# Kernel optimization log

Hardware: AMD Instinct MI355X
Metric: run time of the kernel (lower is better)

## Reference

```python
import jax, jax.numpy as jnp
import numpy as np

B, N, D, C = 2048, 1024, 128, 10  # batch, SOM neurons (32x32), feature dim, classes


def setup_inputs() -> dict:
    key = jax.random.key(0)
    k_x, k_y, k_n, k_l = jax.random.split(key, 4)
    x = jax.random.normal(k_x, (B, D), dtype=jnp.float32)
    y = jax.random.uniform(k_y, (B, C), dtype=jnp.float32)  # argmax -> class ids
    neurons = jax.random.normal(k_n, (N, D), dtype=jnp.float32)
    # labels initialized as random one-hot rows, matching torch one_hot(randint)
    lab_ids = jax.random.randint(k_l, (N,), 0, C)
    labels = jax.nn.one_hot(lab_ids, C, dtype=jnp.float32)
    activities = jnp.zeros((N, C), dtype=jnp.float32)
    labels_count = jnp.zeros((C,), dtype=jnp.int64) if jax.config.jax_enable_x64 else jnp.zeros((C,), dtype=jnp.int32)
    sigma = jnp.ones((1,), dtype=jnp.float32) * 1.5
    return {"x": x, "y": y, "neurons": neurons, "labels": labels,
            "activities": activities, "labels_count": labels_count, "sigma": sigma}


def reference(x, y, neurons, labels, activities, labels_count, sigma):
    sig = sigma[0]
    xr = x.reshape(x.shape[0], 1, -1)              # [B,1,D]
    diff = xr - neurons[None, :, :]                # [B,N,D] broadcasted difference
    d2 = jnp.sum(diff * diff, axis=-1)             # [B,N] squared distances
    d = jnp.sqrt(d2)                               # [B,N]
    bmu = jnp.argmin(d2, axis=-1)                  # [B] best-matching unit
    bmu_d2 = jnp.min(d2, axis=-1)                  # [B]
    g_bmu = jnp.exp(-jnp.sqrt(bmu_d2) / sig)       # [B]
    g = jnp.exp(-d / sig)                          # [B,N]
    gb = g_bmu[:, None]                            # [B,1]
    g_norm = jnp.where(gb == 0, jnp.zeros((), g.dtype), g / gb)  # [B,N]
    batch_last = g_norm.T                          # [N,B] (movedim(0,-1))
    cls = jnp.argmax(y, axis=-1)                   # [B] truth classes
    new_activities = activities.at[:, cls].add(batch_last)   # scatter-add over classes
    new_counts = labels_count.at[cls].add(1)
    out = labels[bmu]                              # [B,C] gather per-sample BMU label
    return out, new_activities, new_counts
```

## Files before the change

kernel.cpp:

```cpp
#include <hip/hip_runtime.h>
#include <hip/hip_bf16.h>
#include <hip/hip_fp16.h>
#include <math.h>

#define Bq 2048
#define Nn 1024
#define Dd 128
#define Cc 10
#define MM 16
#define NBLK (Bq / MM)
#define NTH 1024
#define NC (Nn * Cc)
#define PART_HALFS (NBLK * NC)

#define ACT_OFF (Bq * Cc)
#define CNT_OFF (Bq * Cc + Nn * Cc)

#define WS_CLS_BYTE  (PART_HALFS * 2)
#define WS_NBH_BYTE  (((WS_CLS_BYTE + Bq * 4) + 255) & ~255)
#define WS_NS2_BYTE  (WS_NBH_BYTE + 16 * Nn * 16)
#define WS_NEED_BYTES (WS_NS2_BYTE + Nn * 4)

typedef __attribute__((ext_vector_type(8))) short short8;
typedef __attribute__((ext_vector_type(4))) float f32x4;

__device__ __forceinline__ ushort f2bf(float v, float* back) {
    __hip_bfloat16 h = __float2bfloat16(v);
    *back = __bfloat162float(h);
    return *(const ushort*)&h;
}

__global__ __launch_bounds__(256) void som_prep(
    const float* __restrict__ neurons,
    short8* __restrict__ nbh,
    float* __restrict__ ns2)
{
    __shared__ ushort hsh[8][128];
    const int t     = threadIdx.x;
    const int base8 = blockIdx.x * 8;

    const int r = t >> 5;
    const int c = (t * 4) & 127;
    float4 v = *(const float4*)&neurons[(long)(base8 + r) * Dd + c];
    float back, s;
    ushort h0 = f2bf(v.x, &back); s  = back * back;
    ushort h1 = f2bf(v.y, &back); s += back * back;
    ushort h2 = f2bf(v.z, &back); s += back * back;
    ushort h3 = f2bf(v.w, &back); s += back * back;
    hsh[r][c + 0] = h0;
    hsh[r][c + 1] = h1;
    hsh[r][c + 2] = h2;
    hsh[r][c + 3] = h3;

    #pragma unroll
    for (int off = 16; off; off >>= 1) s += __shfl_xor(s, off);
    if ((t & 31) == 0) ns2[base8 + r] = s;
    __syncthreads();

    if (t < 128) {
        int r2 = t >> 4, kb = t & 15;
        short8 H = *(const short8*)&hsh[r2][kb * 8];
        nbh[kb * Nn + base8 + r2] = H;
    }
}

__global__ __launch_bounds__(NTH) void som_dist(
    const float* __restrict__ x,
    const float* __restrict__ y,
    const short8* __restrict__ nbh,
    const float* __restrict__ ns2,
    const float* __restrict__ labels,
    const float* __restrict__ sigma,
    float* __restrict__ out,
    __half* __restrict__ ws_p,
    int*   __restrict__ ws_cls)
{
    __shared__ ushort xsh[MM * 128];
    __shared__ ushort xsl[MM * 128];
    __shared__ float  xs2s[MM];
    __shared__ float  candv[16][MM];
    __shared__ int    candi[16][MM];
    __shared__ float  bmu_d[MM];
    __shared__ int    bmu_i[MM];
    __shared__ int    clss[MM];

    const int t    = threadIdx.x;
    const int b0   = blockIdx.x * MM;
    const int w    = t >> 6;
    const int lane = t & 63;
    const int g    = lane >> 4;
    const int c16  = lane & 15;

    #pragma unroll
    for (int ii = 0; ii < 2; ++ii) {
        int i   = t + ii * 1024;
        int row = i >> 7;
        int k   = i & 127;
        float v = x[(b0 + row) * Dd + k];
        float back; ushort h = f2bf(v, &back);
        float lo = v - back;
        float b2; ushort l = f2bf(lo, &b2);
        int kb  = k >> 3, j = k & 7;
        int idx = row * 128 + ((kb ^ (row & 7)) << 3) + j;
        xsh[idx] = h;
        xsl[idx] = l;
    }

    {
        float v0 = x[(b0 + w) * Dd + lane];
        float v1 = x[(b0 + w) * Dd + lane + 64];
        float s  = fmaf(v0, v0, v1 * v1);
        #pragma unroll
        for (int off = 32; off; off >>= 1) s += __shfl_xor(s, off);
        if (lane == 0) xs2s[w] = s;
    }
    __syncthreads();

    float dvv[4][4];
    float mval[4]; int midx[4];
    #pragma unroll
    for (int r = 0; r < 4; ++r) { mval[r] = 3.4e38f; midx[r] = 0; }

    const int rowa   = c16;
    const int abase  = rowa * 128;
    const int axor   = (rowa & 7);

    #pragma unroll
    for (int ti = 0; ti < 4; ++ti) {
        const int n0 = w * 64 + ti * 16;
        f32x4 acc = {0.f, 0.f, 0.f, 0.f};
        #pragma unroll
        for (int ks = 0; ks < 4; ++ks) {
            const int kb = ks * 4 + g;
            const int ai = abase + ((kb ^ axor) << 3);
            short8 ah = *(const short8*)&xsh[ai];
            short8 al = *(const short8*)&xsl[ai];
            short8 bh = nbh[kb * Nn + n0 + c16];
            acc = __builtin_amdgcn_mfma_f32_16x16x32_bf16(ah, bh, acc, 0, 0, 0);
            acc = __builtin_amdgcn_mfma_f32_16x16x32_bf16(al, bh, acc, 0, 0, 0);
        }
        const float ns2v = ns2[n0 + c16];
        #pragma unroll
        for (int r = 0; r < 4; ++r) {
            float dv = fmaf(-2.f, acc[r], ns2v);
            dvv[ti][r] = dv;
            if (dv < mval[r]) { mval[r] = dv; midx[r] = n0 + c16; }
        }
    }

    #pragma unroll
    for (int r = 0; r < 4; ++r) {
        float bv = mval[r]; int bi = midx[r];
        #pragma unroll
        for (int off = 8; off; off >>= 1) {
            float ov = __shfl_xor(bv, off);
            int   oi = __shfl_xor(bi, off);
            if (ov < bv || (ov == bv && oi < bi)) { bv = ov; bi = oi; }
        }
        if (c16 == 0) { candv[w][g * 4 + r] = bv; candi[w][g * 4 + r] = bi; }
    }
    __syncthreads();

    if (t < MM) {
        float best = candv[0][t]; int bidx = candi[0][t];
        #pragma unroll
        for (int w2 = 1; w2 < 16; ++w2) {
            float v = candv[w2][t]; int i2 = candi[w2][t];
            if (v < best || (v == best && i2 < bidx)) { best = v; bidx = i2; }
        }
        bmu_i[t] = bidx;
        float d2 = xs2s[t] + best;
        bmu_d[t] = sqrtf(d2 > 0.f ? d2 : 0.f);

        const float* yr = y + (long)(b0 + t) * Cc;
        float bvv = yr[0]; int bc = 0;
        #pragma unroll
        for (int c = 1; c < Cc; ++c) { float v = yr[c]; if (v > bvv) { bvv = v; bc = c; } }
        clss[t] = bc;
        ws_cls[b0 + t] = bc;
    }
    __syncthreads();

    if (t < MM * Cc) {
        int b = t / Cc, c = t % Cc;
        out[(b0 + b) * Cc + c] = labels[bmu_i[b] * Cc + c];
    }

    const float inv_sig = 1.f / sigma[0];
    __half* pb = ws_p + (long)blockIdx.x * NC;

    #pragma unroll
    for (int ti = 0; ti < 4; ++ti) {
        const int n0 = w * 64 + ti * 16;
        float sc[Cc];
        #pragma unroll
        for (int c = 0; c < Cc; ++c) sc[c] = 0.f;
        #pragma unroll
        for (int r = 0; r < 4; ++r) {
            int   row = g * 4 + r;
            float d2  = xs2s[row] + dvv[ti][r];
            float d   = sqrtf(d2 > 0.f ? d2 : 0.f);
            float gn  = expf((bmu_d[row] - d) * inv_sig);
            int   cl  = clss[row];
            #pragma unroll
            for (int c = 0; c < Cc; ++c) sc[c] += (cl == c) ? gn : 0.f;
        }
        #pragma unroll
        for (int c = 0; c < Cc; ++c) {
            float v = sc[c];
            v += __shfl_xor(v, 16);
            v += __shfl_xor(v, 32);
            if (g == 0) pb[c * Nn + n0 + c16] = __float2half(v);
        }
    }
}

__global__ __launch_bounds__(256) void som_fin(
    const float* __restrict__ act_in,
    const int*   __restrict__ cnt_in,
    const __half* __restrict__ ws_p,
    const int*   __restrict__ ws_cls,
    float* __restrict__ out)
{
    if (blockIdx.x < 160) {
        const int t  = threadIdx.x;
        const int kc = t & 3;
        const int j  = blockIdx.x * 64 + (t >> 2);
        const int c  = j >> 10;
        const int n  = j & (Nn - 1);
        const __half* p = ws_p + (long)(kc * 32) * NC + j;
        float s = 0.f;
        #pragma unroll 8
        for (int i = 0; i < 32; ++i) s += __half2float(p[(long)i * NC]);
        s += __shfl_down(s, 2);
        s += __shfl_down(s, 1);
        if (kc == 0) out[ACT_OFF + n * Cc + c] = act_in[n * Cc + c] + s;
    } else {
        __shared__ int hist[Cc];
        if (threadIdx.x < Cc) hist[threadIdx.x] = 0;
        __syncthreads();
        for (int b = threadIdx.x; b < Bq; b += 256) atomicAdd(&hist[ws_cls[b]], 1);
        __syncthreads();
        if (threadIdx.x < Cc)
            out[CNT_OFF + threadIdx.x] = (float)(cnt_in[threadIdx.x] + hist[threadIdx.x]);
    }
}

__global__ void som_init(const float* __restrict__ act_in,
                         const int* __restrict__ cnt_in,
                         float* __restrict__ out) {
    int i = blockIdx.x * blockDim.x + threadIdx.x;
    if (i < Nn * Cc) out[ACT_OFF + i] = act_in[i];
    if (i < Cc) out[CNT_OFF + i] = (float)cnt_in[i];
}

__global__ __launch_bounds__(512) void som_main(
    const float* __restrict__ x,
    const float* __restrict__ y,
    const float* __restrict__ neurons,
    const float* __restrict__ labels,
    const float* __restrict__ sigma,
    float* __restrict__ out)
{
    __shared__ float xs[8][Dd];
    __shared__ float d2s[8][Nn];
    __shared__ float bmu_d[8];
    __shared__ int   bmu_i[8];
    __shared__ int   clss[8];

    const int t  = threadIdx.x;
    const int b0 = blockIdx.x * 8;

    for (int i = t; i < 8 * Dd; i += 512)
        xs[i >> 7][i & (Dd - 1)] = x[b0 * Dd + i];
    __syncthreads();

    float acc0[8], acc1[8];
    #pragma unroll
    for (int b = 0; b < 8; ++b) { acc0[b] = 0.f; acc1[b] = 0.f; }

    const float4* nr0 = (const float4*)(neurons + t * Dd);
    const float4* nr1 = (const float4*)(neurons + (t + 512) * Dd);

    #pragma unroll 2
    for (int dc = 0; dc < Dd / 4; ++dc) {
        float4 nv0 = nr0[dc];
        float4 nv1 = nr1[dc];
        #pragma unroll
        for (int b = 0; b < 8; ++b) {
            float4 xv = *(const float4*)&xs[b][dc * 4];
            float d;
            d = xv.x - nv0.x; acc0[b] = fmaf(d, d, acc0[b]);
            d = xv.y - nv0.y; acc0[b] = fmaf(d, d, acc0[b]);
            d = xv.z - nv0.z; acc0[b] = fmaf(d, d, acc0[b]);
            d = xv.w - nv0.w; acc0[b] = fmaf(d, d, acc0[b]);
            d = xv.x - nv1.x; acc1[b] = fmaf(d, d, acc1[b]);
            d = xv.y - nv1.y; acc1[b] = fmaf(d, d, acc1[b]);
            d = xv.z - nv1.z; acc1[b] = fmaf(d, d, acc1[b]);
            d = xv.w - nv1.w; acc1[b] = fmaf(d, d, acc1[b]);
        }
    }

    #pragma unroll
    for (int b = 0; b < 8; ++b) {
        d2s[b][t]       = acc0[b];
        d2s[b][t + 512] = acc1[b];
    }
    __syncthreads();

    {
        const int wv = t >> 6, lane = t & 63;
        float best = 3.4e38f; int bidx = 0;
        #pragma unroll
        for (int i = 0; i < Nn / 64; ++i) {
            int idx = lane + i * 64;
            float v = d2s[wv][idx];
            if (v < best) { best = v; bidx = idx; }
        }
        #pragma unroll
        for (int off = 32; off; off >>= 1) {
            float ov = __shfl_down(best, off);
            int   oi = __shfl_down(bidx, off);
            if (ov < best || (ov == best && oi < bidx)) { best = ov; bidx = oi; }
        }
        if (lane == 0) { bmu_i[wv] = bidx; bmu_d[wv] = sqrtf(best); }
    }

    if (t < 8) {
        const float* yr = y + (long)(b0 + t) * Cc;
        float bv = yr[0]; int bc = 0;
        #pragma unroll
        for (int c = 1; c < Cc; ++c) { float v = yr[c]; if (v > bv) { bv = v; bc = c; } }
        clss[t] = bc;
        atomicAdd(out + CNT_OFF + bc, 1.0f);
    }
    __syncthreads();

    for (int i = t; i < 8 * Cc; i += 512) {
        int b = i / Cc, c = i % Cc;
        out[(long)(b0 + b) * Cc + c] = labels[(long)bmu_i[b] * Cc + c];
    }

    const float sig = sigma[0];
    #pragma unroll
    for (int b = 0; b < 8; ++b) {
        float gb = expf(-bmu_d[b] / sig);
        int   cl = clss[b];
        float g0 = expf(-sqrtf(acc0[b]) / sig);
        float g1 = expf(-sqrtf(acc1[b]) / sig);
        float gn0 = (gb == 0.f) ? 0.f : g0 / gb;
        float gn1 = (gb == 0.f) ? 0.f : g1 / gb;
        atomicAdd(out + ACT_OFF + t * Cc + cl, gn0);
        atomicAdd(out + ACT_OFF + (t + 512) * Cc + cl, gn1);
    }
}

extern "C" void kernel_launch(void* const* d_in, const int* in_sizes, int n_in,
                              void* d_out, int out_size, void* d_ws, size_t ws_size,
                              hipStream_t stream) {
    const float* x       = (const float*)d_in[0];
    const float* y       = (const float*)d_in[1];
    const float* neurons = (const float*)d_in[2];
    const float* labels  = (const float*)d_in[3];
    const float* act     = (const float*)d_in[4];
    const int*   cnt     = (const int*)d_in[5];
    const float* sigma   = (const float*)d_in[6];
    float* out = (float*)d_out;

    if (ws_size >= (size_t)WS_NEED_BYTES) {
        char*   wsb    = (char*)d_ws;
        __half* ws_p   = (__half*)wsb;
        int*    ws_cls = (int*)(wsb + WS_CLS_BYTE);
        short8* ws_nbh = (short8*)(wsb + WS_NBH_BYTE);
        float*  ws_ns2 = (float*)(wsb + WS_NS2_BYTE);
        som_prep<<<128, 256, 0, stream>>>(neurons, ws_nbh, ws_ns2);
        som_dist<<<NBLK, NTH, 0, stream>>>(x, y, ws_nbh, ws_ns2, labels, sigma, out, ws_p, ws_cls);
        som_fin<<<161, 256, 0, stream>>>(act, cnt, ws_p, ws_cls, out);
    } else {
        som_init<<<(Nn * Cc + 255) / 256, 256, 0, stream>>>(act, cnt, out);
        som_main<<<Bq / 8, 512, 0, stream>>>(x, y, neurons, labels, sigma, out);
    }
}
```

Measured before the change: 30.16 us.

## Fuse prep, distance and reduction kernels into one launch with grid barriers

Merges the three kernels (neuron bf16 conversion, distance/BMU computation, partial-sum reduction) into a single persistent kernel of 128 blocks that synchronises with a software grid barrier built on atomics. The aim is to remove two kernel launch gaps and their tail effects. In exchange it adds a memset launch for the barrier counters, two spin-wait barriers, and relies on all 128 1024-thread blocks being co-resident, which should hold on a 256-CU MI355X. The final reduction is also re-tiled to 640 threads per block with 8-way splits.

```diff
diff --git a/kernel.cpp b/kernel.cpp
--- a/kernel.cpp
+++ b/kernel.cpp
@@ -19,7 +19,8 @@
 #define WS_CLS_BYTE  (PART_HALFS * 2)
 #define WS_NBH_BYTE  (((WS_CLS_BYTE + Bq * 4) + 255) & ~255)
 #define WS_NS2_BYTE  (WS_NBH_BYTE + 16 * Nn * 16)
-#define WS_NEED_BYTES (WS_NS2_BYTE + Nn * 4)
+#define WS_BAR_BYTE  (((WS_NS2_BYTE + Nn * 4) + 15) & ~15)
+#define WS_NEED_BYTES (WS_BAR_BYTE + 16)
 
 typedef __attribute__((ext_vector_type(8))) short short8;
 typedef __attribute__((ext_vector_type(4))) float f32x4;
@@ -30,51 +31,40 @@
     return *(const ushort*)&h;
 }
 
-__global__ __launch_bounds__(256) void som_prep(
-    const float* __restrict__ neurons,
-    short8* __restrict__ nbh,
-    float* __restrict__ ns2)
-{
-    __shared__ ushort hsh[8][128];
-    const int t     = threadIdx.x;
-    const int base8 = blockIdx.x * 8;
-
-    const int r = t >> 5;
-    const int c = (t * 4) & 127;
-    float4 v = *(const float4*)&neurons[(long)(base8 + r) * Dd + c];
-    float back, s;
-    ushort h0 = f2bf(v.x, &back); s  = back * back;
-    ushort h1 = f2bf(v.y, &back); s += back * back;
-    ushort h2 = f2bf(v.z, &back); s += back * back;
-    ushort h3 = f2bf(v.w, &back); s += back * back;
-    hsh[r][c + 0] = h0;
-    hsh[r][c + 1] = h1;
-    hsh[r][c + 2] = h2;
-    hsh[r][c + 3] = h3;
-
-    #pragma unroll
-    for (int off = 16; off; off >>= 1) s += __shfl_xor(s, off);
-    if ((t & 31) == 0) ns2[base8 + r] = s;
-    __syncthreads();
-
-    if (t < 128) {
-        int r2 = t >> 4, kb = t & 15;
-        short8 H = *(const short8*)&hsh[r2][kb * 8];
-        nbh[kb * Nn + base8 + r2] = H;
-    }
-}
-
-__global__ __launch_bounds__(NTH) void som_dist(
+__device__ __forceinline__ void grid_barrier(int* bcnt, int* bgen) {
+    __syncthreads();
+    if (threadIdx.x == 0) {
+        __threadfence();
+        int g = __hip_atomic_load(bgen, __ATOMIC_RELAXED, __HIP_MEMORY_SCOPE_AGENT);
+        if (__hip_atomic_fetch_add(bcnt, 1, __ATOMIC_ACQ_REL, __HIP_MEMORY_SCOPE_AGENT) == NBLK - 1) {
+            __hip_atomic_store(bcnt, 0, __ATOMIC_RELAXED, __HIP_MEMORY_SCOPE_AGENT);
+            __hip_atomic_fetch_add(bgen, 1, __ATOMIC_RELEASE, __HIP_MEMORY_SCOPE_AGENT);
+        } else {
+            while (__hip_atomic_load(bgen, __ATOMIC_ACQUIRE, __HIP_MEMORY_SCOPE_AGENT) == g)
+                __builtin_amdgcn_s_sleep(2);
+        }
+        __threadfence();
+    }
+    __syncthreads();
+}
+
+__global__ __launch_bounds__(NTH) void som_fused(
     const float* __restrict__ x,
     const float* __restrict__ y,
-    const short8* __restrict__ nbh,
-    const float* __restrict__ ns2,
+    const float* __restrict__ neurons,
     const float* __restrict__ labels,
+    const float* __restrict__ act_in,
+    const int*   __restrict__ cnt_in,
     const float* __restrict__ sigma,
     float* __restrict__ out,
     __half* __restrict__ ws_p,
-    int*   __restrict__ ws_cls)
+    int*    __restrict__ ws_cls,
+    short8* __restrict__ nbh,
+    float*  __restrict__ ns2,
+    int* bcnt, int* bgen)
 {
+    __shared__ ushort hsh[8][128];
+    __shared__ float  halfsum[16];
     __shared__ ushort xsh[MM * 128];
     __shared__ ushort xsl[MM * 128];
     __shared__ float  xs2s[MM];
@@ -85,11 +75,25 @@
     __shared__ int    clss[MM];
 
     const int t    = threadIdx.x;
-    const int b0   = blockIdx.x * MM;
+    const int bk   = blockIdx.x;
+    const int b0   = bk * MM;
     const int w    = t >> 6;
     const int lane = t & 63;
     const int g    = lane >> 4;
     const int c16  = lane & 15;
+
+    {
+        const int base8 = bk * 8;
+        const int r = t >> 7;
+        const int c = t & 127;
+        float v = neurons[(base8 + r) * Dd + c];
+        float back; ushort h = f2bf(v, &back);
+        hsh[r][c] = h;
+        float s = back * back;
+        #pragma unroll
+        for (int off = 32; off; off >>= 1) s += __shfl_xor(s, off);
+        if (lane == 0) halfsum[w] = s;
+    }
 
     #pragma unroll
     for (int ii = 0; ii < 2; ++ii) {
@@ -116,14 +120,25 @@
     }
     __syncthreads();
 
+    {
+        const int base8 = bk * 8;
+        if (t < 8) ns2[base8 + t] = halfsum[2 * t] + halfsum[2 * t + 1];
+        if (t < 128) {
+            int r2 = t >> 4, kb = t & 15;
+            nbh[kb * Nn + base8 + r2] = *(const short8*)&hsh[r2][kb * 8];
+        }
+    }
+
+    grid_barrier(bcnt, bgen);
+
     float dvv[4][4];
     float mval[4]; int midx[4];
     #pragma unroll
     for (int r = 0; r < 4; ++r) { mval[r] = 3.4e38f; midx[r] = 0; }
 
-    const int rowa   = c16;
-    const int abase  = rowa * 128;
-    const int axor   = (rowa & 7);
+    const int rowa  = c16;
+    const int abase = rowa * 128;
+    const int axor  = (rowa & 7);
 
     #pragma unroll
     for (int ti = 0; ti < 4; ++ti) {
@@ -187,7 +202,7 @@
     }
 
     const float inv_sig = 1.f / sigma[0];
-    __half* pb = ws_p + (long)blockIdx.x * NC;
+    __half* pb = ws_p + (long)bk * NC;
 
     #pragma unroll
     for (int ti = 0; ti < 4; ++ti) {
@@ -213,36 +228,31 @@
             if (g == 0) pb[c * Nn + n0 + c16] = __float2half(v);
         }
     }
-}
-
-__global__ __launch_bounds__(256) void som_fin(
-    const float* __restrict__ act_in,
-    const int*   __restrict__ cnt_in,
-    const __half* __restrict__ ws_p,
-    const int*   __restrict__ ws_cls,
-    float* __restrict__ out)
-{
-    if (blockIdx.x < 160) {
-        const int t  = threadIdx.x;
-        const int kc = t & 3;
-        const int j  = blockIdx.x * 64 + (t >> 2);
+
+    grid_barrier(bcnt, bgen);
+
+    if (t < 640) {
+        const int kc = t & 7;
+        const int j  = bk * 80 + (t >> 3);
         const int c  = j >> 10;
         const int n  = j & (Nn - 1);
-        const __half* p = ws_p + (long)(kc * 32) * NC + j;
+        const __half* p = ws_p + (long)(kc * 16) * NC + j;
         float s = 0.f;
-        #pragma unroll 8
-        for (int i = 0; i < 32; ++i) s += __half2float(p[(long)i * NC]);
+        #pragma unroll
+        for (int i = 0; i < 16; ++i) s += __half2float(p[(long)i * NC]);
+        s += __shfl_down(s, 4);
         s += __shfl_down(s, 2);
         s += __shfl_down(s, 1);
         if (kc == 0) out[ACT_OFF + n * Cc + c] = act_in[n * Cc + c] + s;
-    } else {
+    }
+
+    if (bk == 0) {
         __shared__ int hist[Cc];
-        if (threadIdx.x < Cc) hist[threadIdx.x] = 0;
+        if (t < Cc) hist[t] = 0;
         __syncthreads();
-        for (int b = threadIdx.x; b < Bq; b += 256) atomicAdd(&hist[ws_cls[b]], 1);
+        for (int b = t; b < Bq; b += NTH) atomicAdd(&hist[ws_cls[b]], 1);
         __syncthreads();
-        if (threadIdx.x < Cc)
-            out[CNT_OFF + threadIdx.x] = (float)(cnt_in[threadIdx.x] + hist[threadIdx.x]);
+        if (t < Cc) out[CNT_OFF + t] = (float)(cnt_in[t] + hist[t]);
     }
 }
 
@@ -373,9 +383,10 @@
         int*    ws_cls = (int*)(wsb + WS_CLS_BYTE);
         short8* ws_nbh = (short8*)(wsb + WS_NBH_BYTE);
         float*  ws_ns2 = (float*)(wsb + WS_NS2_BYTE);
-        som_prep<<<128, 256, 0, stream>>>(neurons, ws_nbh, ws_ns2);
-        som_dist<<<NBLK, NTH, 0, stream>>>(x, y, ws_nbh, ws_ns2, labels, sigma, out, ws_p, ws_cls);
-        som_fin<<<161, 256, 0, stream>>>(act, cnt, ws_p, ws_cls, out);
+        int*    bar    = (int*)(wsb + WS_BAR_BYTE);
+        hipMemsetAsync(bar, 0, 8, stream);
+        som_fused<<<NBLK, NTH, 0, stream>>>(x, y, neurons, labels, act, cnt, sigma, out,
+                                            ws_p, ws_cls, ws_nbh, ws_ns2, bar, bar + 1);
     } else {
         som_init<<<(Nn * Cc + 255) / 256, 256, 0, stream>>>(act, cnt, out);
         som_main<<<Bq / 8, 512, 0, stream>>>(x, y, neurons, labels, sigma, out);
```

After: 56.93 us. 1.89x slower.
